# Kernel optimization log

Measured on AMD Instinct MI355X. Metric: run time of the kernel, lower is better.

Reference implementation:

```python
import jax, jax.numpy as jnp
import numpy as np

B, H, S, D = 2, 16, 2048, 128


def setup_inputs() -> dict:
    key = jax.random.key(0)
    kq, kk, kv = jax.random.split(key, 3)
    q = jax.random.normal(kq, (B, H, S, D), dtype=jnp.float32)
    k = jax.random.normal(kk, (B, H, S, D), dtype=jnp.float32)
    v = jax.random.normal(kv, (B, H, S, D), dtype=jnp.float32)
    scale = jnp.float32(1.0 / np.sqrt(D))
    return {"q": q, "k": k, "v": v, "scale": scale}


def reference(q, k, v, scale):
    # scores: [B, H, S, S]
    attn = jnp.einsum("bhqd,bhkd->bhqk", q, k) * scale
    attn = jnp.square(jax.nn.relu(attn))  # relu(x)^2 score function (no softmax)
    return jnp.einsum("bhqk,bhkd->bhqd", attn, v)
```

## Files before the change

### kernel.cpp

```cpp
#include <hip/hip_runtime.h>
#include <hip/hip_bf16.h>
#include <stdint.h>

#define S_LEN 2048
#define D_DIM 128
#define QT 128
#define KT 64
#define NT (S_LEN/KT)
#define KS 136
#define VS 72
#define PS 72

typedef float  f32x4  __attribute__((ext_vector_type(4)));
typedef short  bf16x8 __attribute__((ext_vector_type(8)));

__device__ __forceinline__ short f2bf(float f) {
    return __builtin_bit_cast(short, __float2bfloat16(f));
}

__global__ __launch_bounds__(256, 2)
void relu2_attn_kernel(const float* __restrict__ q,
                       const float* __restrict__ k,
                       const float* __restrict__ v,
                       const float* __restrict__ scale_p,
                       float* __restrict__ out) {
    __shared__ short Klds[KT][KS];
    __shared__ short VTlds[D_DIM][VS];
    __shared__ short Plds[QT][PS];

    const int tid  = threadIdx.x;
    const int wave = tid >> 6;
    const int lane = tid & 63;
    const int l15  = lane & 15;
    const int lg   = lane >> 4;

    const int bid = blockIdx.x;
    const int bh  = bid & 31;
    const int qt  = bid >> 5;
    const int q0  = qt * QT;

    const float* qb = q + (size_t)bh * S_LEN * D_DIM;
    const float* kb = k + (size_t)bh * S_LEN * D_DIM;
    const float* vb = v + (size_t)bh * S_LEN * D_DIM;
    float*       ob = out + (size_t)bh * S_LEN * D_DIM;

    const float scale = scale_p[0];

    bf16x8 qa[2][4];
    {
        const int qrow = q0 + wave * 32;
        #pragma unroll
        for (int qf = 0; qf < 2; ++qf) {
            const float* qp = qb + (size_t)(qrow + qf*16 + l15) * D_DIM + lg * 8;
            #pragma unroll
            for (int dk = 0; dk < 4; ++dk) {
                f32x4 a = *(const f32x4*)(qp + dk*32);
                f32x4 b = *(const f32x4*)(qp + dk*32 + 4);
                bf16x8 t;
                t[0]=f2bf(a[0]*scale); t[1]=f2bf(a[1]*scale);
                t[2]=f2bf(a[2]*scale); t[3]=f2bf(a[3]*scale);
                t[4]=f2bf(b[0]*scale); t[5]=f2bf(b[1]*scale);
                t[6]=f2bf(b[2]*scale); t[7]=f2bf(b[3]*scale);
                qa[qf][dk] = t;
            }
        }
    }

    const int kr = tid >> 4;
    const int kc = tid & 15;
    const int vd = tid & 127;
    const int vh = (tid >> 7) * 32;

    f32x4 kreg[8];
    float vreg[32];

#define LOAD_TILE(T) do {                                                     \
    const float* kp_ = kb + (size_t)((T) * KT) * D_DIM;                       \
    _Pragma("unroll")                                                         \
    for (int p = 0; p < 4; ++p) {                                             \
        const float* rp_ = kp_ + (size_t)(p*16 + kr) * D_DIM + kc*8;          \
        kreg[2*p]   = *(const f32x4*)rp_;                                     \
        kreg[2*p+1] = *(const f32x4*)(rp_ + 4);                               \
    }                                                                         \
    const float* vp_ = vb + (size_t)((T) * KT + vh) * D_DIM + vd;             \
    _Pragma("unroll")                                                         \
    for (int j = 0; j < 32; ++j) vreg[j] = vp_[(size_t)j * D_DIM];            \
} while (0)

#define STORE_TILE() do {                                                     \
    _Pragma("unroll")                                                         \
    for (int p = 0; p < 4; ++p) {                                             \
        f32x4 a_ = kreg[2*p], b_ = kreg[2*p+1];                               \
        bf16x8 w_;                                                            \
        w_[0]=f2bf(a_[0]); w_[1]=f2bf(a_[1]); w_[2]=f2bf(a_[2]); w_[3]=f2bf(a_[3]); \
        w_[4]=f2bf(b_[0]); w_[5]=f2bf(b_[1]); w_[6]=f2bf(b_[2]); w_[7]=f2bf(b_[3]); \
        *(bf16x8*)&Klds[p*16 + kr][kc*8] = w_;                                \
    }                                                                         \
    _Pragma("unroll")                                                         \
    for (int c = 0; c < 4; ++c) {                                             \
        bf16x8 w_;                                                            \
        w_[0]=f2bf(vreg[c*8+0]); w_[1]=f2bf(vreg[c*8+1]);                     \
        w_[2]=f2bf(vreg[c*8+2]); w_[3]=f2bf(vreg[c*8+3]);                     \
        w_[4]=f2bf(vreg[c*8+4]); w_[5]=f2bf(vreg[c*8+5]);                     \
        w_[6]=f2bf(vreg[c*8+6]); w_[7]=f2bf(vreg[c*8+7]);                     \
        *(bf16x8*)&VTlds[vd][vh + c*8] = w_;                                  \
    }                                                                         \
} while (0)

    f32x4 oacc[2][8];
    #pragma unroll
    for (int i = 0; i < 2; ++i)
        #pragma unroll
        for (int j = 0; j < 8; ++j)
            oacc[i][j] = f32x4{0.f, 0.f, 0.f, 0.f};

    LOAD_TILE(0);

    for (int t = 0; t < NT; ++t) {
        STORE_TILE();
        __syncthreads();

        LOAD_TILE((t + 1) & (NT - 1));

        f32x4 sacc[2][4];
        #pragma unroll
        for (int qf = 0; qf < 2; ++qf)
            #pragma unroll
            for (int kf = 0; kf < 4; ++kf)
                sacc[qf][kf] = f32x4{0.f, 0.f, 0.f, 0.f};

        #pragma unroll
        for (int dk = 0; dk < 4; ++dk) {
            #pragma unroll
            for (int kf = 0; kf < 4; ++kf) {
                bf16x8 bf = *(const bf16x8*)&Klds[kf*16 + l15][dk*32 + lg*8];
                #pragma unroll
                for (int qf = 0; qf < 2; ++qf)
                    sacc[qf][kf] = __builtin_amdgcn_mfma_f32_16x16x32_bf16(
                        qa[qf][dk], bf, sacc[qf][kf], 0, 0, 0);
            }
        }

        #pragma unroll
        for (int qf = 0; qf < 2; ++qf) {
            #pragma unroll
            for (int kf = 0; kf < 4; ++kf) {
                f32x4 sv = sacc[qf][kf];
                #pragma unroll
                for (int e = 0; e < 4; ++e) {
                    float r = fmaxf(sv[e], 0.f);
                    Plds[wave*32 + qf*16 + lg*4 + e][kf*16 + l15] = f2bf(r * r);
                }
            }
        }

        #pragma unroll
        for (int ks = 0; ks < 2; ++ks) {
            bf16x8 pa[2];
            #pragma unroll
            for (int qf = 0; qf < 2; ++qf)
                pa[qf] = *(const bf16x8*)&Plds[wave*32 + qf*16 + l15][ks*32 + lg*8];
            #pragma unroll
            for (int df = 0; df < 8; ++df) {
                bf16x8 vf = *(const bf16x8*)&VTlds[df*16 + l15][ks*32 + lg*8];
                #pragma unroll
                for (int qf = 0; qf < 2; ++qf)
                    oacc[qf][df] = __builtin_amdgcn_mfma_f32_16x16x32_bf16(
                        pa[qf], vf, oacc[qf][df], 0, 0, 0);
            }
        }
        __syncthreads();
    }

    #pragma unroll
    for (int qf = 0; qf < 2; ++qf) {
        #pragma unroll
        for (int df = 0; df < 8; ++df) {
            f32x4 o = oacc[qf][df];
            const int row = q0 + wave*32 + qf*16 + lg*4;
            float* op = ob + (size_t)row * D_DIM + df*16 + l15;
            op[0*D_DIM] = o[0];
            op[1*D_DIM] = o[1];
            op[2*D_DIM] = o[2];
            op[3*D_DIM] = o[3];
        }
    }
}

extern "C" void kernel_launch(void* const* d_in, const int* in_sizes, int n_in,
                              void* d_out, int out_size, void* d_ws, size_t ws_size,
                              hipStream_t stream) {
    const float* q = (const float*)d_in[0];
    const float* k = (const float*)d_in[1];
    const float* v = (const float*)d_in[2];
    const float* scale = (const float*)d_in[3];
    float* out = (float*)d_out;

    const int blocks = (2 * 16) * (S_LEN / QT);
    relu2_attn_kernel<<<dim3(blocks), dim3(256), 0, stream>>>(q, k, v, scale, out);
}
```

Measured before the change: 103.3 us.

## Pre-convert K and transpose V to bf16, stream tiles via direct global-to-LDS loads

Adds two prepass kernels that convert K to bf16 and write V transposed in bf16 into the workspace. The main kernel then double-buffers K/V tiles into LDS with global_load_lds and XOR-swizzled layouts, instead of per-iteration fp32 register loads, conversion and LDS stores. It also swaps MFMA operand order so P can be written as bf16x4 vectors. This targets the repeated fp32 conversion work and halves the per-tile bytes each block reads, at the cost of two extra launches and a workspace round trip. The old kernel is kept as a fallback when the workspace is too small.

```diff
diff --git a/kernel.cpp b/kernel.cpp
--- a/kernel.cpp
+++ b/kernel.cpp
@@ -7,38 +7,247 @@
 #define QT 128
 #define KT 64
 #define NT (S_LEN/KT)
-#define KS 136
-#define VS 72
-#define PS 72
 
 typedef float  f32x4  __attribute__((ext_vector_type(4)));
 typedef short  bf16x8 __attribute__((ext_vector_type(8)));
+typedef short  bf16x4 __attribute__((ext_vector_type(4)));
 
 __device__ __forceinline__ short f2bf(float f) {
     return __builtin_bit_cast(short, __float2bfloat16(f));
 }
 
+__device__ __forceinline__ void gload_lds16(const short* g, short* l) {
+    __builtin_amdgcn_global_load_lds(
+        (const __attribute__((address_space(1))) void*)g,
+        (__attribute__((address_space(3))) void*)l,
+        16, 0, 0);
+}
+
+__global__ __launch_bounds__(256)
+void convert_k_kernel(const float* __restrict__ kin, short* __restrict__ kbf) {
+    const size_t i = ((size_t)blockIdx.x * 256 + threadIdx.x) * 8;
+    f32x4 a = *(const f32x4*)(kin + i);
+    f32x4 c = *(const f32x4*)(kin + i + 4);
+    bf16x8 t;
+    t[0]=f2bf(a[0]); t[1]=f2bf(a[1]); t[2]=f2bf(a[2]); t[3]=f2bf(a[3]);
+    t[4]=f2bf(c[0]); t[5]=f2bf(c[1]); t[6]=f2bf(c[2]); t[7]=f2bf(c[3]);
+    *(bf16x8*)(kbf + i) = t;
+}
+
+__global__ __launch_bounds__(256)
+void transpose_v_kernel(const float* __restrict__ vin, short* __restrict__ vt) {
+    __shared__ short T[16 * 130];
+    const int tid = threadIdx.x;
+    const int blk = blockIdx.x;
+    const int bh  = blk >> 3;
+    const int d0  = (blk & 7) * 16;
+    const float* vb = vin + (size_t)bh * S_LEN * D_DIM;
+    short* vtb = vt + (size_t)bh * (size_t)D_DIM * S_LEN;
+    const int c4 = tid & 3;
+    const int rr = tid >> 2;
+    const int dl = tid >> 4;
+    const int kc = tid & 15;
+
+    for (int kc0 = 0; kc0 < S_LEN; kc0 += 128) {
+        #pragma unroll
+        for (int h = 0; h < 2; ++h) {
+            const int krow = kc0 + h*64 + rr;
+            f32x4 a = *(const f32x4*)(vb + (size_t)krow * D_DIM + d0 + c4*4);
+            #pragma unroll
+            for (int j = 0; j < 4; ++j)
+                T[(c4*4 + j)*130 + h*64 + rr] = f2bf(a[j]);
+        }
+        __syncthreads();
+        int w0 = *(const int*)&T[dl*130 + kc*8 + 0];
+        int w1 = *(const int*)&T[dl*130 + kc*8 + 2];
+        int w2 = *(const int*)&T[dl*130 + kc*8 + 4];
+        int w3 = *(const int*)&T[dl*130 + kc*8 + 6];
+        int4 val = make_int4(w0, w1, w2, w3);
+        *(int4*)(vtb + (size_t)(d0 + dl) * S_LEN + kc0 + kc*8) = val;
+        __syncthreads();
+    }
+}
+
+#define KOFF(B) ((B)*8192)
+#define VOFF(B) (16384 + (B)*8192)
+#define POFF 32768
+
 __global__ __launch_bounds__(256, 2)
-void relu2_attn_kernel(const float* __restrict__ q,
-                       const float* __restrict__ k,
-                       const float* __restrict__ v,
-                       const float* __restrict__ scale_p,
-                       float* __restrict__ out) {
-    __shared__ short Klds[KT][KS];
-    __shared__ short VTlds[D_DIM][VS];
-    __shared__ short Plds[QT][PS];
+void relu2_attn_main(const float* __restrict__ q,
+                     const short* __restrict__ kbf,
+                     const short* __restrict__ vtbf,
+                     const float* __restrict__ scale_p,
+                     float* __restrict__ out) {
+    __shared__ short lds[40960];
 
     const int tid  = threadIdx.x;
     const int wave = tid >> 6;
     const int lane = tid & 63;
     const int l15  = lane & 15;
     const int lg   = lane >> 4;
+    const int swz  = l15 & 7;
 
     const int bid = blockIdx.x;
     const int bh  = bid & 31;
     const int qt  = bid >> 5;
     const int q0  = qt * QT;
 
+    const float* qb = q    + (size_t)bh * S_LEN * D_DIM;
+    const short* kb = kbf  + (size_t)bh * S_LEN * D_DIM;
+    const short* vt = vtbf + (size_t)bh * (size_t)D_DIM * S_LEN;
+    float*       ob = out  + (size_t)bh * S_LEN * D_DIM;
+
+    const float scale = scale_p[0];
+
+    bf16x8 qa[2][4];
+    {
+        const int qrow = q0 + wave * 32;
+        #pragma unroll
+        for (int qf = 0; qf < 2; ++qf) {
+            const float* qp = qb + (size_t)(qrow + qf*16 + l15) * D_DIM + lg * 8;
+            #pragma unroll
+            for (int dk = 0; dk < 4; ++dk) {
+                f32x4 a = *(const f32x4*)(qp + dk*32);
+                f32x4 c = *(const f32x4*)(qp + dk*32 + 4);
+                bf16x8 t;
+                t[0]=f2bf(a[0]*scale); t[1]=f2bf(a[1]*scale);
+                t[2]=f2bf(a[2]*scale); t[3]=f2bf(a[3]*scale);
+                t[4]=f2bf(c[0]*scale); t[5]=f2bf(c[1]*scale);
+                t[6]=f2bf(c[2]*scale); t[7]=f2bf(c[3]*scale);
+                qa[qf][dk] = t;
+            }
+        }
+    }
+
+    f32x4 oacc[2][8];
+    #pragma unroll
+    for (int i = 0; i < 2; ++i)
+        #pragma unroll
+        for (int j = 0; j < 8; ++j)
+            oacc[i][j] = f32x4{0.f, 0.f, 0.f, 0.f};
+
+#define STAGE(T, B) do {                                                      \
+    const int k0_ = (T) * KT;                                                 \
+    _Pragma("unroll")                                                         \
+    for (int p_ = 0; p_ < 4; ++p_) {                                          \
+        const int ch_ = p_*4 + wave;                                          \
+        const int r_  = ch_*4 + (lane >> 4);                 \
+        gload_lds16(kb + (((size_t)(k0_ + r_)) << 7)                          \
+                       + (((lane & 15) ^ (r_ & 7)) << 3),                     \
+                    &lds[KOFF(B) + ch_*512]);                                 \
+        const int d_  = ch_*8 + (lane >> 3);            \
+        gload_lds16(vt + (((size_t)d_) << 11) + k0_                           \
+                       + (((lane & 7) ^ (d_ & 7)) << 3),                      \
+                    &lds[VOFF(B) + ch_*512]);                                 \
+    }                                                                         \
+} while (0)
+
+    STAGE(0, 0);
+
+    for (int t = 0; t < NT; ++t) {
+        const int b = t & 1;
+        __syncthreads();
+        if (t + 1 < NT) STAGE(t + 1, b ^ 1);
+
+        f32x4 sacc[2][4];
+        #pragma unroll
+        for (int qf = 0; qf < 2; ++qf)
+            #pragma unroll
+            for (int kf = 0; kf < 4; ++kf)
+                sacc[qf][kf] = f32x4{0.f, 0.f, 0.f, 0.f};
+
+        #pragma unroll
+        for (int dk = 0; dk < 4; ++dk) {
+            #pragma unroll
+            for (int kf = 0; kf < 4; ++kf) {
+                const int krow = kf*16 + l15;
+                bf16x8 af = *(const bf16x8*)
+                    &lds[KOFF(b) + krow*128 + (((dk*4 + lg) ^ swz) << 3)];
+                #pragma unroll
+                for (int qf = 0; qf < 2; ++qf)
+                    sacc[qf][kf] = __builtin_amdgcn_mfma_f32_16x16x32_bf16(
+                        af, qa[qf][dk], sacc[qf][kf], 0, 0, 0);
+            }
+        }
+
+        #pragma unroll
+        for (int qf = 0; qf < 2; ++qf) {
+            const int qrow = wave*32 + qf*16 + l15;
+            #pragma unroll
+            for (int kf = 0; kf < 4; ++kf) {
+                f32x4 sv = sacc[qf][kf];
+                bf16x4 w;
+                #pragma unroll
+                for (int e = 0; e < 4; ++e) {
+                    float r0 = fmaxf(sv[e], 0.f);
+                    w[e] = f2bf(r0 * r0);
+                }
+                *(bf16x4*)&lds[POFF + qrow*64 + ((kf*16 + lg*4) ^ (swz << 3))] = w;
+            }
+        }
+
+        #pragma unroll
+        for (int ks = 0; ks < 2; ++ks) {
+            bf16x8 pa[2];
+            #pragma unroll
+            for (int qf = 0; qf < 2; ++qf) {
+                const int qrow = wave*32 + qf*16 + l15;
+                pa[qf] = *(const bf16x8*)
+                    &lds[POFF + qrow*64 + ((ks*32 + lg*8) ^ (swz << 3))];
+            }
+            #pragma unroll
+            for (int df = 0; df < 8; ++df) {
+                const int drow = df*16 + l15;
+                bf16x8 vf = *(const bf16x8*)
+                    &lds[VOFF(b) + drow*64 + (((ks*4 + lg) ^ swz) << 3)];
+                #pragma unroll
+                for (int qf = 0; qf < 2; ++qf)
+                    oacc[qf][df] = __builtin_amdgcn_mfma_f32_16x16x32_bf16(
+                        pa[qf], vf, oacc[qf][df], 0, 0, 0);
+            }
+        }
+    }
+
+    #pragma unroll
+    for (int qf = 0; qf < 2; ++qf) {
+        #pragma unroll
+        for (int df = 0; df < 8; ++df) {
+            f32x4 o = oacc[qf][df];
+            const int row = q0 + wave*32 + qf*16 + lg*4;
+            float* op = ob + (size_t)row * D_DIM + df*16 + l15;
+            op[0*D_DIM] = o[0];
+            op[1*D_DIM] = o[1];
+            op[2*D_DIM] = o[2];
+            op[3*D_DIM] = o[3];
+        }
+    }
+}
+
+#define KS 136
+#define VS 72
+#define PS 72
+
+__global__ __launch_bounds__(256, 2)
+void relu2_attn_fallback(const float* __restrict__ q,
+                         const float* __restrict__ k,
+                         const float* __restrict__ v,
+                         const float* __restrict__ scale_p,
+                         float* __restrict__ out) {
+    __shared__ short Klds[KT][KS];
+    __shared__ short VTlds[D_DIM][VS];
+    __shared__ short Plds[QT][PS];
+
+    const int tid  = threadIdx.x;
+    const int wave = tid >> 6;
+    const int lane = tid & 63;
+    const int l15  = lane & 15;
+    const int lg   = lane >> 4;
+
+    const int bid = blockIdx.x;
+    const int bh  = bid & 31;
+    const int qt  = bid >> 5;
+    const int q0  = qt * QT;
+
     const float* qb = q + (size_t)bh * S_LEN * D_DIM;
     const float* kb = k + (size_t)bh * S_LEN * D_DIM;
     const float* vb = v + (size_t)bh * S_LEN * D_DIM;
@@ -55,12 +264,12 @@
             #pragma unroll
             for (int dk = 0; dk < 4; ++dk) {
                 f32x4 a = *(const f32x4*)(qp + dk*32);
-                f32x4 b = *(const f32x4*)(qp + dk*32 + 4);
+                f32x4 c = *(const f32x4*)(qp + dk*32 + 4);
                 bf16x8 t;
                 t[0]=f2bf(a[0]*scale); t[1]=f2bf(a[1]*scale);
                 t[2]=f2bf(a[2]*scale); t[3]=f2bf(a[3]*scale);
-                t[4]=f2bf(b[0]*scale); t[5]=f2bf(b[1]*scale);
-                t[6]=f2bf(b[2]*scale); t[7]=f2bf(b[3]*scale);
+                t[4]=f2bf(c[0]*scale); t[5]=f2bf(c[1]*scale);
+                t[6]=f2bf(c[2]*scale); t[7]=f2bf(c[3]*scale);
                 qa[qf][dk] = t;
             }
         }
@@ -74,7 +283,7 @@
     f32x4 kreg[8];
     float vreg[32];
 
-#define LOAD_TILE(T) do {                                                     \
+#define FLOAD_TILE(T) do {                                                    \
     const float* kp_ = kb + (size_t)((T) * KT) * D_DIM;                       \
     _Pragma("unroll")                                                         \
     for (int p = 0; p < 4; ++p) {                                             \
@@ -87,7 +296,7 @@
     for (int j = 0; j < 32; ++j) vreg[j] = vp_[(size_t)j * D_DIM];            \
 } while (0)
 
-#define STORE_TILE() do {                                                     \
+#define FSTORE_TILE() do {                                                    \
     _Pragma("unroll")                                                         \
     for (int p = 0; p < 4; ++p) {                                             \
         f32x4 a_ = kreg[2*p], b_ = kreg[2*p+1];                               \
@@ -114,13 +323,12 @@
         for (int j = 0; j < 8; ++j)
             oacc[i][j] = f32x4{0.f, 0.f, 0.f, 0.f};
 
-    LOAD_TILE(0);
+    FLOAD_TILE(0);
 
     for (int t = 0; t < NT; ++t) {
-        STORE_TILE();
+        FSTORE_TILE();
         __syncthreads();
-
-        LOAD_TILE((t + 1) & (NT - 1));
+        FLOAD_TILE((t + 1) & (NT - 1));
 
         f32x4 sacc[2][4];
         #pragma unroll
@@ -196,6 +404,16 @@
     const float* scale = (const float*)d_in[3];
     float* out = (float*)d_out;
 
-    const int blocks = (2 * 16) * (S_LEN / QT);
-    relu2_attn_kernel<<<dim3(blocks), dim3(256), 0, stream>>>(q, k, v, scale, out);
-}
+    const size_t elems = (size_t)2 * 16 * S_LEN * D_DIM;
+    const size_t need  = elems * 2 * 2;
+
+    if (ws_size >= need) {
+        short* kbf = (short*)d_ws;
+        short* vtb = (short*)d_ws + elems;
+        convert_k_kernel<<<dim3((int)(elems / (256 * 8))), dim3(256), 0, stream>>>(k, kbf);
+        transpose_v_kernel<<<dim3(256), dim3(256), 0, stream>>>(v, vtb);
+        relu2_attn_main<<<dim3(512), dim3(256), 0, stream>>>(q, kbf, vtb, scale, out);
+    } else {
+        relu2_attn_fallback<<<dim3(512), dim3(256), 0, stream>>>(q, k, v, scale, out);
+    }
+}
```

After: 97.94 us. -5.2%, faster.
